# Optimization experiments

Hardware: AMD Instinct MI355X
Metric: run time of the kernel (lower is better)

## Reference

```python
import jax, jax.numpy as jnp
import numpy as np

NH = 16   # n_heads
HD = 64   # head_size
EMB = 1024  # n_embd = NH * HD
B, T = 4, 2048


def setup_inputs() -> dict:
    key = jax.random.key(0)
    k1, k2, k3 = jax.random.split(key, 3)
    x = jax.random.normal(k1, (B, T, EMB), dtype=jnp.float32)
    # torch Linear(in, out, bias=False): weight [out,in]; we store transposed [in,out]
    W_attn = jax.random.normal(k2, (EMB, 3 * NH * HD), dtype=jnp.float32) * (EMB ** -0.5)
    W_proj = jax.random.normal(k3, (NH * HD, EMB), dtype=jnp.float32) * ((NH * HD) ** -0.5)
    b_proj = jnp.zeros((EMB,), dtype=jnp.float32)
    return {"x": x, "W_attn": W_attn, "W_proj": W_proj, "b_proj": b_proj}


def reference(x, W_attn, W_proj, b_proj):
    Bq, Tq, C = x.shape
    qkv = x @ W_attn                      # [B,T,3*Nh*H]
    qs, ks, vs = jnp.split(qkv, 3, axis=2)
    def to_heads(t):                      # [B,T,Nh*H] -> [B,Nh,T,H]
        return t.reshape(Bq, Tq, NH, HD).transpose(0, 2, 1, 3)
    q, k, v = to_heads(qs), to_heads(ks), to_heads(vs)
    scores = jnp.einsum('bnth,bnsh->bnts', q, k) * (HD ** -0.5)  # [B,Nh,T,T]
    causal = jnp.tril(jnp.ones((Tq, Tq), dtype=bool))
    scores = jnp.where(causal, scores, -jnp.inf)
    attn = jax.nn.softmax(scores, axis=-1)
    # dropout is identity in eval mode
    y = jnp.einsum('bnts,bnsh->bnth', attn, v)                   # [B,Nh,T,H]
    y = y.transpose(0, 2, 1, 3).reshape(Bq, Tq, NH * HD)
    return y @ W_proj + b_proj
```

## Files before the change

### kernel.cpp

```cpp
#include <hip/hip_runtime.h>
#include <hip/hip_bf16.h>

#define NH 16
#define HD 64
#define EMB 1024
#define BB 4
#define TT 2048
#define MTOT (BB*TT)
#define N1 (3*NH*HD)
#define KD EMB

#define QSCALE 0.18033688011112042f
#define FMAX 14.0f

typedef __bf16 bf16x8 __attribute__((ext_vector_type(8)));
typedef __bf16 bf16x4 __attribute__((ext_vector_type(4)));
typedef float  f32x4  __attribute__((ext_vector_type(4)));
typedef __hip_bfloat16 hbf;

__device__ __forceinline__ void async_copy16(const hbf* g, hbf* l) {
    __builtin_amdgcn_global_load_lds(
        (const __attribute__((address_space(1))) void*)g,
        (__attribute__((address_space(3))) void*)l, 16, 0, 0);
}

__device__ __forceinline__ bf16x4 pack4(float x0, float x1, float x2, float x3) {
    union { bf16x4 v; hbf a[4]; } u;
    u.a[0] = __float2bfloat16(x0);
    u.a[1] = __float2bfloat16(x1);
    u.a[2] = __float2bfloat16(x2);
    u.a[3] = __float2bfloat16(x3);
    return u.v;
}


__global__ __launch_bounds__(256) void f32_to_bf16_v4(const float* __restrict__ in,
                                                      hbf* __restrict__ out, int n4) {
    int i = blockIdx.x * blockDim.x + threadIdx.x;
    if (i < n4) {
        float4 v = ((const float4*)in)[i];
        *(bf16x4*)(out + 4 * (size_t)i) = pack4(v.x, v.y, v.z, v.w);
    }
}

__global__ __launch_bounds__(256) void f32_to_bf16_T(const float* __restrict__ in,
                                                     hbf* __restrict__ out, int R, int C) {
    __shared__ float T[64][65];
    int bc = blockIdx.x % (C / 64), br = blockIdx.x / (C / 64);
    int r0 = br * 64, c0 = bc * 64;
    int tr = threadIdx.x >> 6, tc = threadIdx.x & 63;
    #pragma unroll
    for (int i = 0; i < 16; ++i)
        T[4 * i + tr][tc] = in[(size_t)(r0 + 4 * i + tr) * C + c0 + tc];
    __syncthreads();
    #pragma unroll
    for (int i = 0; i < 16; ++i)
        out[(size_t)(c0 + 4 * i + tr) * R + r0 + tc] = __float2bfloat16(T[tc][4 * i + tr]);
}


template<int NBN, int MODE>
__global__ __launch_bounds__(512, 4) void gemm8(
    const hbf* __restrict__ A, const hbf* __restrict__ Bt,
    hbf* __restrict__ qh, hbf* __restrict__ kh, hbf* __restrict__ vt,
    const float* __restrict__ bias, float* __restrict__ out)
{
    constexpr int NKT = KD / 64;
    __shared__ __align__(16) hbf As[2 * 128 * 64];
    __shared__ __align__(16) hbf Bs[2 * 128 * 64];

    int tid = threadIdx.x;
    int wv = tid >> 6, lane = tid & 63;
    int g = lane >> 4, c = lane & 15;
    int wm = wv >> 2, wn = wv & 3;
    int bn = blockIdx.x % NBN, bm = blockIdx.x / NBN;
    int m0 = bm * 128, n0 = bn * 128;

    int sr0 = tid >> 3;
    int sgc = (tid & 7) ^ (sr0 & 7);
    const hbf* Asrc0 = A  + (size_t)(m0 + sr0) * KD + sgc * 8;
    const hbf* Asrc1 = A  + (size_t)(m0 + 64 + sr0) * KD + sgc * 8;
    const hbf* Bsrc0 = Bt + (size_t)(n0 + sr0) * KD + sgc * 8;
    const hbf* Bsrc1 = Bt + (size_t)(n0 + 64 + sr0) * KD + sgc * 8;
    int ldst0 = (tid & ~63) * 8;
    int ldst1 = 4096 + (tid & ~63) * 8;

#define STAGE_A8(tt, buf) { async_copy16(Asrc0 + (tt) * 64, As + (buf) * 8192 + ldst0); \
                            async_copy16(Asrc1 + (tt) * 64, As + (buf) * 8192 + ldst1); }
#define STAGE_B8(tt, buf) { async_copy16(Bsrc0 + (tt) * 64, Bs + (buf) * 8192 + ldst0); \
                            async_copy16(Bsrc1 + (tt) * 64, Bs + (buf) * 8192 + ldst1); }

    int xr = c & 7;
    int aoff0 = (wm * 64 + c) * 64 + ((g ^ xr) << 3);
    int aoff1 = (wm * 64 + c) * 64 + (((4 + g) ^ xr) << 3);
    int boff0 = (wn * 32 + c) * 64 + ((g ^ xr) << 3);
    int boff1 = (wn * 32 + c) * 64 + (((4 + g) ^ xr) << 3);

    f32x4 acc[4][2];
    #pragma unroll
    for (int i = 0; i < 4; ++i)
        #pragma unroll
        for (int j = 0; j < 2; ++j) acc[i][j] = (f32x4){0.f, 0.f, 0.f, 0.f};

    STAGE_A8(0, 0);
    STAGE_B8(0, 0);
    STAGE_A8(1, 1);
    asm volatile("s_waitcnt vmcnt(2)" ::: "memory");
    asm volatile("s_barrier" ::: "memory");
    __builtin_amdgcn_sched_barrier(0);

    for (int t = 0; t < NKT; ++t) {
        int cur = t & 1;
        const hbf* Ab = As + cur * 8192;
        const hbf* Bb = Bs + cur * 8192;
        bf16x8 af[4][2], bfr[2];
        #pragma unroll
        for (int i = 0; i < 4; ++i) {
            af[i][0] = *(const bf16x8*)(Ab + aoff0 + i * 1024);
            af[i][1] = *(const bf16x8*)(Ab + aoff1 + i * 1024);
        }
        bfr[0] = *(const bf16x8*)(Bb + boff0);
        bfr[1] = *(const bf16x8*)(Bb + boff1);
        if (t + 1 < NKT) STAGE_B8(t + 1, cur ^ 1);
        __builtin_amdgcn_s_setprio(1);
        #pragma unroll
        for (int i = 0; i < 4; ++i) {
            acc[i][0] = __builtin_amdgcn_mfma_f32_16x16x32_bf16(af[i][0], bfr[0], acc[i][0], 0, 0, 0);
            acc[i][0] = __builtin_amdgcn_mfma_f32_16x16x32_bf16(af[i][1], bfr[1], acc[i][0], 0, 0, 0);
        }
        __builtin_amdgcn_s_setprio(0);
        asm volatile("s_barrier" ::: "memory");
        __builtin_amdgcn_sched_barrier(0);
        bfr[0] = *(const bf16x8*)(Bb + boff0 + 1024);
        bfr[1] = *(const bf16x8*)(Bb + boff1 + 1024);
        if (t + 2 < NKT) STAGE_A8(t + 2, cur);
        __builtin_amdgcn_s_setprio(1);
        #pragma unroll
        for (int i = 0; i < 4; ++i) {
            acc[i][1] = __builtin_amdgcn_mfma_f32_16x16x32_bf16(af[i][0], bfr[0], acc[i][1], 0, 0, 0);
            acc[i][1] = __builtin_amdgcn_mfma_f32_16x16x32_bf16(af[i][1], bfr[1], acc[i][1], 0, 0, 0);
        }
        __builtin_amdgcn_s_setprio(0);
        if (t + 2 < NKT) { asm volatile("s_waitcnt vmcnt(2)" ::: "memory"); }
        else             { asm volatile("s_waitcnt vmcnt(0)" ::: "memory"); }
        asm volatile("s_barrier" ::: "memory");
        __builtin_amdgcn_sched_barrier(0);
    }

#undef STAGE_A8
#undef STAGE_B8

    if constexpr (MODE == 0) {
        int colbase = n0 + wn * 32;
        int which = colbase >> 10;
        int h = (colbase & 1023) >> 6;
        int dbase = colbase & 63;
        int b = m0 / TT;
        int trow = (m0 % TT) + wm * 64;
        if (which < 2) {
            float scale = (which == 0) ? QSCALE : 1.0f;
            hbf* dst = ((which == 0) ? qh : kh) + ((size_t)b * NH + h) * TT * HD;
            #pragma unroll
            for (int i = 0; i < 4; ++i)
                #pragma unroll
                for (int nf = 0; nf < 2; ++nf) {
                    int d = dbase + nf * 16 + c;
                    #pragma unroll
                    for (int r = 0; r < 4; ++r) {
                        int trw = trow + i * 16 + g * 4 + r;
                        dst[(size_t)trw * HD + d] = __float2bfloat16(acc[i][nf][r] * scale);
                    }
                }
        } else {
            hbf* dst = vt + ((size_t)b * NH + h) * TT * HD;
            #pragma unroll
            for (int i = 0; i < 4; ++i)
                #pragma unroll
                for (int nf = 0; nf < 2; ++nf) {
                    int d = dbase + nf * 16 + c;
                    #pragma unroll
                    for (int r = 0; r < 4; ++r) {
                        int trw = trow + i * 16 + g * 4 + r;
                        dst[(size_t)d * TT + trw] = __float2bfloat16(acc[i][nf][r]);
                    }
                }
        }
    } else {
        #pragma unroll
        for (int i = 0; i < 4; ++i)
            #pragma unroll
            for (int nf = 0; nf < 2; ++nf) {
                int col = n0 + wn * 32 + nf * 16 + c;
                float bv = bias[col];
                #pragma unroll
                for (int r = 0; r < 4; ++r) {
                    int row = m0 + wm * 64 + i * 16 + g * 4 + r;
                    out[(size_t)row * EMB + col] = acc[i][nf][r] + bv;
                }
            }
    }
}


__global__ __launch_bounds__(512, 4) void attn(
    const hbf* __restrict__ qh, const hbf* __restrict__ kh, const hbf* __restrict__ vt,
    hbf* __restrict__ y)
{
    __shared__ __align__(16) hbf Ks[128 * 64];
    __shared__ __align__(16) hbf Vs[64 * 128];
    __shared__ __align__(16) hbf Ps[8][16 * 64];

    int tid = threadIdx.x;
    int wv = tid >> 6, lane = tid & 63;
    int g = lane >> 4, c = lane & 15;
    int c7 = c & 7;

    int bh = blockIdx.x >> 3;
    int pi = blockIdx.x & 7;
    int b = bh >> 4, h = bh & 15;

    const hbf* Q = qh + (size_t)bh * TT * HD;
    const hbf* K = kh + (size_t)bh * TT * HD;
    const hbf* V = vt + (size_t)bh * TT * HD;
    hbf* Pq = &Ps[wv][0];

    union { bf16x8 v; hbf a[8]; } uo;
    #pragma unroll
    for (int i = 0; i < 8; ++i) uo.a[i] = __float2bfloat16(1.0f);
    const bf16x8 ones8 = uo.v;

    #pragma unroll
    for (int pass = 0; pass < 2; ++pass) {
        int sst = pass ? (15 - pi) : pi;
        int qb = sst * 128;
        int q0 = qb + wv * 16;
        int kend = q0 + 16;
        int kmax = qb + 128;

        bf16x8 aq0 = *(const bf16x8*)(Q + (size_t)(q0 + c) * HD + g * 8);
        bf16x8 aq1 = *(const bf16x8*)(Q + (size_t)(q0 + c) * HD + 32 + g * 8);

        f32x4 lacc = (f32x4){0.f, 0.f, 0.f, 0.f};
        f32x4 o[4];
        #pragma unroll
        for (int d = 0; d < 4; ++d) o[d] = (f32x4){0.f, 0.f, 0.f, 0.f};

        for (int k0 = 0; k0 < kmax; k0 += 128) {
            __syncthreads();
            #pragma unroll
            for (int it = 0; it < 2; ++it) {
                int e = it * 4096 + tid * 8;
                int key = e >> 6, sblk = (e >> 3) & 7;
                int dblk = sblk ^ (key & 7);
                async_copy16(K + (size_t)(k0 + key) * HD + dblk * 8,
                             Ks + it * 4096 + (tid & ~63) * 8);
            }
            #pragma unroll
            for (int it = 0; it < 2; ++it) {
                int e = it * 4096 + tid * 8;
                int dim = e >> 7, kb = (e >> 3) & 15;
                int skb = kb ^ (dim & 7);
                async_copy16(V + (size_t)dim * TT + k0 + skb * 8,
                             Vs + it * 4096 + (tid & ~63) * 8);
            }
            __syncthreads();

            #pragma unroll
            for (int ch = 0; ch < 2; ++ch) {
                int c64 = k0 + ch * 64;
                if (c64 < kend) {
                    f32x4 s[4];
                    #pragma unroll
                    for (int t = 0; t < 4; ++t) {
                        int kt = c64 + 16 * t;
                        if (kt < kend) {
                            int rb = (ch * 64 + 16 * t + c) * 64;
                            bf16x8 kf0 = *(const bf16x8*)(Ks + rb + ((g ^ c7) << 3));
                            bf16x8 kf1 = *(const bf16x8*)(Ks + rb + (((4 + g) ^ c7) << 3));
                            f32x4 a = (f32x4){-FMAX, -FMAX, -FMAX, -FMAX};
                            a = __builtin_amdgcn_mfma_f32_16x16x32_bf16(kf0, aq0, a, 0, 0, 0);
                            a = __builtin_amdgcn_mfma_f32_16x16x32_bf16(kf1, aq1, a, 0, 0, 0);
                            if (kt == q0) {
                                #pragma unroll
                                for (int r = 0; r < 4; ++r)
                                    a[r] = (g * 4 + r <= c) ? a[r] : -1e30f;
                            }
                            s[t] = a;
                        } else
                            s[t] = (f32x4){-1e30f, -1e30f, -1e30f, -1e30f};
                    }
                    #pragma unroll
                    for (int t = 0; t < 4; ++t) {
                        f32x4 e;
                        #pragma unroll
                        for (int r = 0; r < 4; ++r) e[r] = __builtin_amdgcn_exp2f(s[t][r]);
                        *(bf16x4*)(Pq + c * 64 + (((2 * t + (g >> 1)) ^ c7) << 3) + ((g & 1) << 2)) =
                            pack4(e[0], e[1], e[2], e[3]);
                    }
                    #pragma unroll
                    for (int sc = 0; sc < 2; ++sc) {
                        if (c64 + 32 * sc < kend) {
                            bf16x8 pf = *(const bf16x8*)(Pq + c * 64 + (((4 * sc + g) ^ c7) << 3));
                            lacc = __builtin_amdgcn_mfma_f32_16x16x32_bf16(ones8, pf, lacc, 0, 0, 0);
                            #pragma unroll
                            for (int d = 0; d < 4; ++d) {
                                int dim = d * 16 + c;
                                bf16x8 vf = *(const bf16x8*)(Vs + dim * 128 +
                                              (((ch * 8 + 4 * sc + g) ^ c7) << 3));
                                o[d] = __builtin_amdgcn_mfma_f32_16x16x32_bf16(vf, pf, o[d], 0, 0, 0);
                            }
                        }
                    }
                }
            }
        }

        float inv = 1.0f / lacc[0];
        #pragma unroll
        for (int d = 0; d < 4; ++d) {
            *(bf16x4*)(y + (size_t)(b * TT + q0 + c) * EMB + h * HD + d * 16 + g * 4) =
                pack4(o[d][0] * inv, o[d][1] * inv, o[d][2] * inv, o[d][3] * inv);
        }
    }
}


extern "C" void kernel_launch(void* const* d_in, const int* in_sizes, int n_in,
                              void* d_out, int out_size, void* d_ws, size_t ws_size,
                              hipStream_t stream)
{
    const float* x      = (const float*)d_in[0];
    const float* W_attn = (const float*)d_in[1];
    const float* W_proj = (const float*)d_in[2];
    const float* b_proj = (const float*)d_in[3];
    float* out = (float*)d_out;

    char* ws = (char*)d_ws;
    hbf* xb    = (hbf*)ws; ws += (size_t)MTOT * KD * 2;
    hbf* wab_t = (hbf*)ws; ws += (size_t)N1 * KD * 2;
    hbf* wpb_t = (hbf*)ws; ws += (size_t)EMB * EMB * 2;
    hbf* qh    = (hbf*)ws; ws += (size_t)MTOT * EMB * 2;
    hbf* kh    = (hbf*)ws; ws += (size_t)MTOT * EMB * 2;
    hbf* vt    = (hbf*)ws; ws += (size_t)MTOT * EMB * 2;
    hbf* yb    = (hbf*)ws; ws += (size_t)MTOT * EMB * 2;

    f32_to_bf16_v4<<<(MTOT * KD / 4 + 255) / 256, 256, 0, stream>>>(x, xb, MTOT * KD / 4);
    f32_to_bf16_T<<<(KD / 64) * (N1 / 64), 256, 0, stream>>>(W_attn, wab_t, KD, N1);
    f32_to_bf16_T<<<(KD / 64) * (EMB / 64), 256, 0, stream>>>(W_proj, wpb_t, KD, EMB);

    gemm8<N1 / 128, 0><<<(MTOT / 128) * (N1 / 128), 512, 0, stream>>>(
        xb, wab_t, qh, kh, vt, nullptr, nullptr);
    attn<<<BB * NH * 8, 512, 0, stream>>>(qh, kh, vt, yb);
    gemm8<EMB / 128, 1><<<(MTOT / 128) * (EMB / 128), 512, 0, stream>>>(
        yb, wpb_t, nullptr, nullptr, nullptr, b_proj, out);
}
```

Measured before the change: 254.2 us.

## Rework GEMM tiling with 4-wave 64x64 warp tiles and double-buffered attention

The GEMM moves to 256 threads with each wave computing a 64x64 tile over K-steps of 32. It uses a simpler single-barrier double buffer and remaps blocks so that consecutive blocks are spread across XCDs. The attention kernel drops its two paired passes per block and instead launches one block per 128-query stripe, heaviest stripes first, with 64-key K/V tiles double-buffered asynchronously and a higher occupancy hint. Together these aim for better register-level reuse and better overlap of loads with MFMA work, at the risk of more register pressure and more barriers per K step.

```diff
diff --git a/kernel.cpp b/kernel.cpp
--- a/kernel.cpp
+++ b/kernel.cpp
@@ -60,101 +60,85 @@
 
 
 template<int NBN, int MODE>
-__global__ __launch_bounds__(512, 4) void gemm8(
+__global__ __launch_bounds__(256, 4) void gemm_v2(
     const hbf* __restrict__ A, const hbf* __restrict__ Bt,
     hbf* __restrict__ qh, hbf* __restrict__ kh, hbf* __restrict__ vt,
     const float* __restrict__ bias, float* __restrict__ out)
 {
-    constexpr int NKT = KD / 64;
-    __shared__ __align__(16) hbf As[2 * 128 * 64];
-    __shared__ __align__(16) hbf Bs[2 * 128 * 64];
+    constexpr int NKT = KD / 32;
+    __shared__ __align__(16) hbf As[2 * 128 * 32];
+    __shared__ __align__(16) hbf Bs[2 * 128 * 32];
 
     int tid = threadIdx.x;
     int wv = tid >> 6, lane = tid & 63;
     int g = lane >> 4, c = lane & 15;
-    int wm = wv >> 2, wn = wv & 3;
-    int bn = blockIdx.x % NBN, bm = blockIdx.x / NBN;
+    int wm = wv >> 1, wn = wv & 1;
+    int wg = (blockIdx.x & 7) * (8 * NBN) + (blockIdx.x >> 3);
+    int bn = wg % NBN, bm = wg / NBN;
     int m0 = bm * 128, n0 = bn * 128;
 
-    int sr0 = tid >> 3;
-    int sgc = (tid & 7) ^ (sr0 & 7);
-    const hbf* Asrc0 = A  + (size_t)(m0 + sr0) * KD + sgc * 8;
-    const hbf* Asrc1 = A  + (size_t)(m0 + 64 + sr0) * KD + sgc * 8;
-    const hbf* Bsrc0 = Bt + (size_t)(n0 + sr0) * KD + sgc * 8;
-    const hbf* Bsrc1 = Bt + (size_t)(n0 + 64 + sr0) * KD + sgc * 8;
-    int ldst0 = (tid & ~63) * 8;
-    int ldst1 = 4096 + (tid & ~63) * 8;
-
-#define STAGE_A8(tt, buf) { async_copy16(Asrc0 + (tt) * 64, As + (buf) * 8192 + ldst0); \
-                            async_copy16(Asrc1 + (tt) * 64, As + (buf) * 8192 + ldst1); }
-#define STAGE_B8(tt, buf) { async_copy16(Bsrc0 + (tt) * 64, Bs + (buf) * 8192 + ldst0); \
-                            async_copy16(Bsrc1 + (tt) * 64, Bs + (buf) * 8192 + ldst1); }
-
-    int xr = c & 7;
-    int aoff0 = (wm * 64 + c) * 64 + ((g ^ xr) << 3);
-    int aoff1 = (wm * 64 + c) * 64 + (((4 + g) ^ xr) << 3);
-    int boff0 = (wn * 32 + c) * 64 + ((g ^ xr) << 3);
-    int boff1 = (wn * 32 + c) * 64 + (((4 + g) ^ xr) << 3);
-
-    f32x4 acc[4][2];
+    int sr = tid >> 2;
+    int sgc = (tid & 3) ^ (sr & 3);
+    const hbf* Asrc0 = A  + (size_t)(m0 + sr) * KD + sgc * 8;
+    const hbf* Asrc1 = A  + (size_t)(m0 + 64 + sr) * KD + sgc * 8;
+    const hbf* Bsrc0 = Bt + (size_t)(n0 + sr) * KD + sgc * 8;
+    const hbf* Bsrc1 = Bt + (size_t)(n0 + 64 + sr) * KD + sgc * 8;
+    int ld0 = (tid & ~63) * 8, ld1 = 2048 + (tid & ~63) * 8;
+
+#define STG(tt, buf) { \
+    async_copy16(Asrc0 + (tt) * 32, As + (buf) * 4096 + ld0); \
+    async_copy16(Asrc1 + (tt) * 32, As + (buf) * 4096 + ld1); \
+    async_copy16(Bsrc0 + (tt) * 32, Bs + (buf) * 4096 + ld0); \
+    async_copy16(Bsrc1 + (tt) * 32, Bs + (buf) * 4096 + ld1); }
+
+    int x3 = c & 3;
+    int ao = (wm * 64 + c) * 32 + ((g ^ x3) << 3);
+    int bo = (wn * 64 + c) * 32 + ((g ^ x3) << 3);
+
+    f32x4 acc[4][4];
     #pragma unroll
     for (int i = 0; i < 4; ++i)
         #pragma unroll
-        for (int j = 0; j < 2; ++j) acc[i][j] = (f32x4){0.f, 0.f, 0.f, 0.f};
-
-    STAGE_A8(0, 0);
-    STAGE_B8(0, 0);
-    STAGE_A8(1, 1);
-    asm volatile("s_waitcnt vmcnt(2)" ::: "memory");
+        for (int j = 0; j < 4; ++j) acc[i][j] = (f32x4){0.f, 0.f, 0.f, 0.f};
+
+    STG(0, 0);
+    STG(1, 1);
+    asm volatile("s_waitcnt vmcnt(4)" ::: "memory");
     asm volatile("s_barrier" ::: "memory");
     __builtin_amdgcn_sched_barrier(0);
 
     for (int t = 0; t < NKT; ++t) {
         int cur = t & 1;
-        const hbf* Ab = As + cur * 8192;
-        const hbf* Bb = Bs + cur * 8192;
-        bf16x8 af[4][2], bfr[2];
-        #pragma unroll
-        for (int i = 0; i < 4; ++i) {
-            af[i][0] = *(const bf16x8*)(Ab + aoff0 + i * 1024);
-            af[i][1] = *(const bf16x8*)(Ab + aoff1 + i * 1024);
-        }
-        bfr[0] = *(const bf16x8*)(Bb + boff0);
-        bfr[1] = *(const bf16x8*)(Bb + boff1);
-        if (t + 1 < NKT) STAGE_B8(t + 1, cur ^ 1);
+        const hbf* Ab = As + cur * 4096;
+        const hbf* Bb = Bs + cur * 4096;
+        bf16x8 af[4], bfr[4];
+        #pragma unroll
+        for (int i = 0; i < 4; ++i) af[i] = *(const bf16x8*)(Ab + ao + i * 512);
+        #pragma unroll
+        for (int j = 0; j < 4; ++j) bfr[j] = *(const bf16x8*)(Bb + bo + j * 512);
+        asm volatile("s_waitcnt lgkmcnt(0)" ::: "memory");
+        __builtin_amdgcn_sched_barrier(0);
+        asm volatile("s_barrier" ::: "memory");
+        __builtin_amdgcn_sched_barrier(0);
+        if (t + 2 < NKT) STG(t + 2, cur);
         __builtin_amdgcn_s_setprio(1);
         #pragma unroll
-        for (int i = 0; i < 4; ++i) {
-            acc[i][0] = __builtin_amdgcn_mfma_f32_16x16x32_bf16(af[i][0], bfr[0], acc[i][0], 0, 0, 0);
-            acc[i][0] = __builtin_amdgcn_mfma_f32_16x16x32_bf16(af[i][1], bfr[1], acc[i][0], 0, 0, 0);
-        }
+        for (int i = 0; i < 4; ++i)
+            #pragma unroll
+            for (int j = 0; j < 4; ++j)
+                acc[i][j] = __builtin_amdgcn_mfma_f32_16x16x32_bf16(af[i], bfr[j], acc[i][j], 0, 0, 0);
         __builtin_amdgcn_s_setprio(0);
-        asm volatile("s_barrier" ::: "memory");
-        __builtin_amdgcn_sched_barrier(0);
-        bfr[0] = *(const bf16x8*)(Bb + boff0 + 1024);
-        bfr[1] = *(const bf16x8*)(Bb + boff1 + 1024);
-        if (t + 2 < NKT) STAGE_A8(t + 2, cur);
-        __builtin_amdgcn_s_setprio(1);
-        #pragma unroll
-        for (int i = 0; i < 4; ++i) {
-            acc[i][1] = __builtin_amdgcn_mfma_f32_16x16x32_bf16(af[i][0], bfr[0], acc[i][1], 0, 0, 0);
-            acc[i][1] = __builtin_amdgcn_mfma_f32_16x16x32_bf16(af[i][1], bfr[1], acc[i][1], 0, 0, 0);
-        }
-        __builtin_amdgcn_s_setprio(0);
-        if (t + 2 < NKT) { asm volatile("s_waitcnt vmcnt(2)" ::: "memory"); }
+        if (t + 2 < NKT) { asm volatile("s_waitcnt vmcnt(4)" ::: "memory"); }
         else             { asm volatile("s_waitcnt vmcnt(0)" ::: "memory"); }
         asm volatile("s_barrier" ::: "memory");
         __builtin_amdgcn_sched_barrier(0);
     }
-
-#undef STAGE_A8
-#undef STAGE_B8
+#undef STG
 
     if constexpr (MODE == 0) {
-        int colbase = n0 + wn * 32;
+        int colbase = n0 + wn * 64;
         int which = colbase >> 10;
         int h = (colbase & 1023) >> 6;
-        int dbase = colbase & 63;
         int b = m0 / TT;
         int trow = (m0 % TT) + wm * 64;
         if (which < 2) {
@@ -163,12 +147,12 @@
             #pragma unroll
             for (int i = 0; i < 4; ++i)
                 #pragma unroll
-                for (int nf = 0; nf < 2; ++nf) {
-                    int d = dbase + nf * 16 + c;
+                for (int j = 0; j < 4; ++j) {
+                    int d = j * 16 + c;
                     #pragma unroll
                     for (int r = 0; r < 4; ++r) {
                         int trw = trow + i * 16 + g * 4 + r;
-                        dst[(size_t)trw * HD + d] = __float2bfloat16(acc[i][nf][r] * scale);
+                        dst[(size_t)trw * HD + d] = __float2bfloat16(acc[i][j][r] * scale);
                     }
                 }
         } else {
@@ -176,12 +160,12 @@
             #pragma unroll
             for (int i = 0; i < 4; ++i)
                 #pragma unroll
-                for (int nf = 0; nf < 2; ++nf) {
-                    int d = dbase + nf * 16 + c;
+                for (int j = 0; j < 4; ++j) {
+                    int d = j * 16 + c;
                     #pragma unroll
                     for (int r = 0; r < 4; ++r) {
                         int trw = trow + i * 16 + g * 4 + r;
-                        dst[(size_t)d * TT + trw] = __float2bfloat16(acc[i][nf][r]);
+                        dst[(size_t)d * TT + trw] = __float2bfloat16(acc[i][j][r]);
                     }
                 }
         }
@@ -189,25 +173,25 @@
         #pragma unroll
         for (int i = 0; i < 4; ++i)
             #pragma unroll
-            for (int nf = 0; nf < 2; ++nf) {
-                int col = n0 + wn * 32 + nf * 16 + c;
+            for (int j = 0; j < 4; ++j) {
+                int col = n0 + wn * 64 + j * 16 + c;
                 float bv = bias[col];
                 #pragma unroll
                 for (int r = 0; r < 4; ++r) {
                     int row = m0 + wm * 64 + i * 16 + g * 4 + r;
-                    out[(size_t)row * EMB + col] = acc[i][nf][r] + bv;
+                    out[(size_t)row * EMB + col] = acc[i][j][r] + bv;
                 }
             }
     }
 }
 
 
-__global__ __launch_bounds__(512, 4) void attn(
+__global__ __launch_bounds__(512, 6) void attn(
     const hbf* __restrict__ qh, const hbf* __restrict__ kh, const hbf* __restrict__ vt,
     hbf* __restrict__ y)
 {
-    __shared__ __align__(16) hbf Ks[128 * 64];
-    __shared__ __align__(16) hbf Vs[64 * 128];
+    __shared__ __align__(16) hbf Ks[2 * 64 * 64];
+    __shared__ __align__(16) hbf Vs[2 * 64 * 64];
     __shared__ __align__(16) hbf Ps[8][16 * 64];
 
     int tid = threadIdx.x;
@@ -215,112 +199,112 @@
     int g = lane >> 4, c = lane & 15;
     int c7 = c & 7;
 
-    int bh = blockIdx.x >> 3;
-    int pi = blockIdx.x & 7;
+    int bidx = blockIdx.x;
+    int bh = (bidx & 7) | (((bidx >> 7) & 7) << 3);
+    int sst = 15 - ((bidx >> 3) & 15);
     int b = bh >> 4, h = bh & 15;
+    int qb = sst * 128;
+    int q0 = qb + wv * 16;
+    int kend = q0 + 16;
+    int nt = 2 * sst + 2;
 
     const hbf* Q = qh + (size_t)bh * TT * HD;
     const hbf* K = kh + (size_t)bh * TT * HD;
     const hbf* V = vt + (size_t)bh * TT * HD;
     hbf* Pq = &Ps[wv][0];
 
+    int skey = tid >> 3, schunk = tid & 7;
+    int sswz = (schunk ^ (skey & 7)) * 8;
+    const hbf* Ksrc = K + (size_t)skey * HD + sswz;
+    const hbf* Vsrc = V + (size_t)skey * TT + sswz;
+    int sdst = (tid & ~63) * 8;
+
+#define ASTG(tt, buf) { \
+    async_copy16(Ksrc + (size_t)(tt) * 64 * HD, Ks + (buf) * 4096 + sdst); \
+    async_copy16(Vsrc + (tt) * 64, Vs + (buf) * 4096 + sdst); }
+
+    bf16x8 aq0 = *(const bf16x8*)(Q + (size_t)(q0 + c) * HD + g * 8);
+    bf16x8 aq1 = *(const bf16x8*)(Q + (size_t)(q0 + c) * HD + 32 + g * 8);
+
     union { bf16x8 v; hbf a[8]; } uo;
     #pragma unroll
     for (int i = 0; i < 8; ++i) uo.a[i] = __float2bfloat16(1.0f);
     const bf16x8 ones8 = uo.v;
 
-    #pragma unroll
-    for (int pass = 0; pass < 2; ++pass) {
-        int sst = pass ? (15 - pi) : pi;
-        int qb = sst * 128;
-        int q0 = qb + wv * 16;
-        int kend = q0 + 16;
-        int kmax = qb + 128;
-
-        bf16x8 aq0 = *(const bf16x8*)(Q + (size_t)(q0 + c) * HD + g * 8);
-        bf16x8 aq1 = *(const bf16x8*)(Q + (size_t)(q0 + c) * HD + 32 + g * 8);
-
-        f32x4 lacc = (f32x4){0.f, 0.f, 0.f, 0.f};
-        f32x4 o[4];
-        #pragma unroll
-        for (int d = 0; d < 4; ++d) o[d] = (f32x4){0.f, 0.f, 0.f, 0.f};
-
-        for (int k0 = 0; k0 < kmax; k0 += 128) {
-            __syncthreads();
-            #pragma unroll
-            for (int it = 0; it < 2; ++it) {
-                int e = it * 4096 + tid * 8;
-                int key = e >> 6, sblk = (e >> 3) & 7;
-                int dblk = sblk ^ (key & 7);
-                async_copy16(K + (size_t)(k0 + key) * HD + dblk * 8,
-                             Ks + it * 4096 + (tid & ~63) * 8);
+    f32x4 lacc = (f32x4){0.f, 0.f, 0.f, 0.f};
+    f32x4 o[4];
+    #pragma unroll
+    for (int d = 0; d < 4; ++d) o[d] = (f32x4){0.f, 0.f, 0.f, 0.f};
+
+    ASTG(0, 0);
+    ASTG(1, 1);
+    asm volatile("s_waitcnt vmcnt(2)" ::: "memory");
+    asm volatile("s_barrier" ::: "memory");
+    __builtin_amdgcn_sched_barrier(0);
+
+    for (int tt = 0; tt < nt; ++tt) {
+        int cur = tt & 1;
+        int k0 = tt * 64;
+        const hbf* Kb = Ks + cur * 4096;
+        const hbf* Vb = Vs + cur * 4096;
+        if (k0 < kend) {
+            f32x4 s[4];
+            #pragma unroll
+            for (int t4 = 0; t4 < 4; ++t4) {
+                int kt = k0 + 16 * t4;
+                if (kt < kend) {
+                    int rb = (16 * t4 + c) * 64;
+                    bf16x8 kf0 = *(const bf16x8*)(Kb + rb + ((g ^ c7) << 3));
+                    bf16x8 kf1 = *(const bf16x8*)(Kb + rb + (((4 + g) ^ c7) << 3));
+                    f32x4 a = (f32x4){-FMAX, -FMAX, -FMAX, -FMAX};
+                    a = __builtin_amdgcn_mfma_f32_16x16x32_bf16(kf0, aq0, a, 0, 0, 0);
+                    a = __builtin_amdgcn_mfma_f32_16x16x32_bf16(kf1, aq1, a, 0, 0, 0);
+                    if (kt == q0) {
+                        #pragma unroll
+                        for (int r = 0; r < 4; ++r)
+                            a[r] = (g * 4 + r <= c) ? a[r] : -1e30f;
+                    }
+                    s[t4] = a;
+                } else
+                    s[t4] = (f32x4){-1e30f, -1e30f, -1e30f, -1e30f};
             }
             #pragma unroll
-            for (int it = 0; it < 2; ++it) {
-                int e = it * 4096 + tid * 8;
-                int dim = e >> 7, kb = (e >> 3) & 15;
-                int skb = kb ^ (dim & 7);
-                async_copy16(V + (size_t)dim * TT + k0 + skb * 8,
-                             Vs + it * 4096 + (tid & ~63) * 8);
+            for (int t4 = 0; t4 < 4; ++t4) {
+                f32x4 e;
+                #pragma unroll
+                for (int r = 0; r < 4; ++r) e[r] = __builtin_amdgcn_exp2f(s[t4][r]);
+                *(bf16x4*)(Pq + c * 64 + (((2 * t4 + (g >> 1)) ^ c7) << 3) + ((g & 1) << 2)) =
+                    pack4(e[0], e[1], e[2], e[3]);
             }
-            __syncthreads();
-
-            #pragma unroll
-            for (int ch = 0; ch < 2; ++ch) {
-                int c64 = k0 + ch * 64;
-                if (c64 < kend) {
-                    f32x4 s[4];
+            #pragma unroll
+            for (int sc = 0; sc < 2; ++sc) {
+                if (k0 + 32 * sc < kend) {
+                    bf16x8 pf = *(const bf16x8*)(Pq + c * 64 + (((4 * sc + g) ^ c7) << 3));
+                    lacc = __builtin_amdgcn_mfma_f32_16x16x32_bf16(ones8, pf, lacc, 0, 0, 0);
                     #pragma unroll
-                    for (int t = 0; t < 4; ++t) {
-                        int kt = c64 + 16 * t;
-                        if (kt < kend) {
-                            int rb = (ch * 64 + 16 * t + c) * 64;
-                            bf16x8 kf0 = *(const bf16x8*)(Ks + rb + ((g ^ c7) << 3));
-                            bf16x8 kf1 = *(const bf16x8*)(Ks + rb + (((4 + g) ^ c7) << 3));
-                            f32x4 a = (f32x4){-FMAX, -FMAX, -FMAX, -FMAX};
-                            a = __builtin_amdgcn_mfma_f32_16x16x32_bf16(kf0, aq0, a, 0, 0, 0);
-                            a = __builtin_amdgcn_mfma_f32_16x16x32_bf16(kf1, aq1, a, 0, 0, 0);
-                            if (kt == q0) {
-                                #pragma unroll
-                                for (int r = 0; r < 4; ++r)
-                                    a[r] = (g * 4 + r <= c) ? a[r] : -1e30f;
-                            }
-                            s[t] = a;
-                        } else
-                            s[t] = (f32x4){-1e30f, -1e30f, -1e30f, -1e30f};
-                    }
-                    #pragma unroll
-                    for (int t = 0; t < 4; ++t) {
-                        f32x4 e;
-                        #pragma unroll
-                        for (int r = 0; r < 4; ++r) e[r] = __builtin_amdgcn_exp2f(s[t][r]);
-                        *(bf16x4*)(Pq + c * 64 + (((2 * t + (g >> 1)) ^ c7) << 3) + ((g & 1) << 2)) =
-                            pack4(e[0], e[1], e[2], e[3]);
-                    }
-                    #pragma unroll
-                    for (int sc = 0; sc < 2; ++sc) {
-                        if (c64 + 32 * sc < kend) {
-                            bf16x8 pf = *(const bf16x8*)(Pq + c * 64 + (((4 * sc + g) ^ c7) << 3));
-                            lacc = __builtin_amdgcn_mfma_f32_16x16x32_bf16(ones8, pf, lacc, 0, 0, 0);
-                            #pragma unroll
-                            for (int d = 0; d < 4; ++d) {
-                                int dim = d * 16 + c;
-                                bf16x8 vf = *(const bf16x8*)(Vs + dim * 128 +
-                                              (((ch * 8 + 4 * sc + g) ^ c7) << 3));
-                                o[d] = __builtin_amdgcn_mfma_f32_16x16x32_bf16(vf, pf, o[d], 0, 0, 0);
-                            }
-                        }
+                    for (int d = 0; d < 4; ++d) {
+                        bf16x8 vf = *(const bf16x8*)(Vb + (d * 16 + c) * 64 +
+                                      (((4 * sc + g) ^ c7) << 3));
+                        o[d] = __builtin_amdgcn_mfma_f32_16x16x32_bf16(vf, pf, o[d], 0, 0, 0);
                     }
                 }
             }
         }
-
-        float inv = 1.0f / lacc[0];
-        #pragma unroll
-        for (int d = 0; d < 4; ++d) {
-            *(bf16x4*)(y + (size_t)(b * TT + q0 + c) * EMB + h * HD + d * 16 + g * 4) =
-                pack4(o[d][0] * inv, o[d][1] * inv, o[d][2] * inv, o[d][3] * inv);
-        }
+        asm volatile("s_barrier" ::: "memory");
+        __builtin_amdgcn_sched_barrier(0);
+        if (tt + 2 < nt) ASTG(tt + 2, cur);
+        if (tt + 2 < nt) { asm volatile("s_waitcnt vmcnt(2)" ::: "memory"); }
+        else             { asm volatile("s_waitcnt vmcnt(0)" ::: "memory"); }
+        asm volatile("s_barrier" ::: "memory");
+        __builtin_amdgcn_sched_barrier(0);
+    }
+#undef ASTG
+
+    float inv = 1.0f / lacc[0];
+    #pragma unroll
+    for (int d = 0; d < 4; ++d) {
+        *(bf16x4*)(y + (size_t)(b * TT + q0 + c) * EMB + h * HD + d * 16 + g * 4) =
+            pack4(o[d][0] * inv, o[d][1] * inv, o[d][2] * inv, o[d][3] * inv);
     }
 }
 
@@ -348,9 +332,9 @@
     f32_to_bf16_T<<<(KD / 64) * (N1 / 64), 256, 0, stream>>>(W_attn, wab_t, KD, N1);
     f32_to_bf16_T<<<(KD / 64) * (EMB / 64), 256, 0, stream>>>(W_proj, wpb_t, KD, EMB);
 
-    gemm8<N1 / 128, 0><<<(MTOT / 128) * (N1 / 128), 512, 0, stream>>>(
+    gemm_v2<N1 / 128, 0><<<(MTOT / 128) * (N1 / 128), 256, 0, stream>>>(
         xb, wab_t, qh, kh, vt, nullptr, nullptr);
-    attn<<<BB * NH * 8, 512, 0, stream>>>(qh, kh, vt, yb);
-    gemm8<EMB / 128, 1><<<(MTOT / 128) * (EMB / 128), 512, 0, stream>>>(
+    attn<<<BB * NH * 16, 512, 0, stream>>>(qh, kh, vt, yb);
+    gemm_v2<EMB / 128, 1><<<(MTOT / 128) * (EMB / 128), 256, 0, stream>>>(
         yb, wpb_t, nullptr, nullptr, nullptr, b_proj, out);
 }
```

Result: slower. 266.8 us (+5.0%).
